# Optimization experiments

Hardware: AMD Instinct MI355X
Metric: run time of the kernel (lower is better)

## Reference

```python
import jax, jax.numpy as jnp
import numpy as np

N = 300_000      # active voxels
L = 128          # occupied bounding grid side
M = 32           # unet width m
CIN = 3          # input_feature_number
NCLASS = 20
K = 27           # 3x3x3 submanifold kernel
BLOCK_REPS = 2
BN_EPS = 1e-4


def _build_neighbors(rng):
    """Rulebook: for each active voxel, index of each of its 27 neighbors (N = missing)."""
    coords = rng.integers(0, L, size=(int(N * 1.5), 3), dtype=np.int64)
    keys = coords[:, 0] * L * L + coords[:, 1] * L + coords[:, 2]
    keys = np.unique(keys)[:N]
    assert keys.shape[0] == N
    x = keys // (L * L); y = (keys // L) % L; z = keys % L
    c = np.stack([x, y, z], 1)                      # [N,3] sorted-by-key coords
    nbr = np.full((N, K), N, dtype=np.int32)
    k = 0
    for dx in (-1, 0, 1):
        for dy in (-1, 0, 1):
            for dz in (-1, 0, 1):
                nc = c + np.array([dx, dy, dz])
                valid = ((nc >= 0) & (nc < L)).all(1)
                nk = nc[:, 0] * L * L + nc[:, 1] * L + nc[:, 2]
                pos = np.searchsorted(keys, nk).clip(0, N - 1)
                found = valid & (keys[pos] == nk)
                nbr[:, k] = np.where(found, pos, N).astype(np.int32)
                k += 1
    return nbr


def setup_inputs() -> dict:
    rng = np.random.default_rng(0)
    nbr_idx = jnp.asarray(_build_neighbors(rng))
    key = jax.random.key(0)
    ks = jax.random.split(key, 16)
    s = 0.1
    inp = {
        "features": jax.random.normal(ks[0], (N, CIN), jnp.float32),
        "nbr_idx": nbr_idx,
        # initial SubmanifoldConvolution(3, m, 3, bias=False)
        "w0": jax.random.normal(ks[1], (K, CIN, M), jnp.float32) * s,
        # residual tower params: [rep, conv_in_block(2), ...]
        "bw": jax.random.normal(ks[2], (BLOCK_REPS, 2, K, M, M), jnp.float32) * s,
        "bg": jnp.ones((BLOCK_REPS, 2, M), jnp.float32),
        "bb": jnp.zeros((BLOCK_REPS, 2, M), jnp.float32),
        # final BatchNormReLU(m)
        "gf": jnp.ones((M,), jnp.float32),
        "bf": jnp.zeros((M,), jnp.float32),
        # dense heads
        "w_cls": jax.random.normal(ks[3], (M, NCLASS), jnp.float32) * s,
        "b_cls": jnp.zeros((NCLASS,), jnp.float32),
        "w_fe": jax.random.normal(ks[4], (M, M), jnp.float32) * s,
        "b_fe": jnp.zeros((M,), jnp.float32),
        "w_le": jax.random.normal(ks[5], (M, M), jnp.float32) * s,
        "b_le": jnp.zeros((M,), jnp.float32),
        "w_fr": jax.random.normal(ks[6], (M, M), jnp.float32) * s,
        "b_fr": jnp.zeros((M,), jnp.float32),
        "w_lr": jax.random.normal(ks[7], (M, 1), jnp.float32) * s,
        "b_lr": jnp.zeros((1,), jnp.float32),
    }
    return inp


def _subconv(feat, nbr, W):
    # feat [N,Cin], nbr [N,27] with sentinel N -> zero row, W [27,Cin,Cout]
    fpad = jnp.concatenate([feat, jnp.zeros((1, feat.shape[1]), feat.dtype)], 0)
    gathered = fpad[nbr]                       # [N,27,Cin] irregular gather
    return jnp.einsum('nkc,kcd->nd', gathered, W)


def _bn(x, g, b):
    mu = x.mean(0)
    var = ((x - mu) ** 2).mean(0)
    return (x - mu) * jax.lax.rsqrt(var + BN_EPS) * g + b


def reference(features, nbr_idx, w0, bw, bg, bb, gf, bf,
              w_cls, b_cls, w_fe, b_fe, w_le, b_le, w_fr, b_fr, w_lr, b_lr):
    feat = _subconv(features, nbr_idx, w0)     # [N,M]
    for r in range(BLOCK_REPS):                # pre-activation residual blocks
        h = _subconv(jax.nn.relu(_bn(feat, bg[r, 0], bb[r, 0])), nbr_idx, bw[r, 0])
        h = _subconv(jax.nn.relu(_bn(h, bg[r, 1], bb[r, 1])), nbr_idx, bw[r, 1])
        feat = feat + h
    feat = jax.nn.relu(_bn(feat, gf, bf))      # BatchNormReLU(m) + OutputLayer
    y = feat @ w_cls + b_cls                                   # [N,20]
    embedding = (feat @ w_fe + b_fe) @ w_le + b_le             # [N,32]
    offset = jax.nn.sigmoid((feat @ w_fr + b_fr) @ w_lr + b_lr)  # [N,1]
    return (y, embedding, offset)
```

## Files before the change

### kernel.cpp

```cpp
#include <hip/hip_runtime.h>

#define NVOX 300000
#define K27 27

typedef __attribute__((ext_vector_type(8))) __bf16 bf16x8;
typedef __attribute__((ext_vector_type(8))) unsigned short ushort8;
typedef __attribute__((ext_vector_type(4))) float f32x4;

__device__ inline unsigned short f2bf(float x){
  unsigned int u = __float_as_uint(x);
  unsigned int r = (u + 0x7FFFu + ((u >> 16) & 1u)) >> 16;
  return (unsigned short)r;
}

__global__ void pack_w_kernel(const float* __restrict__ bw, unsigned short* __restrict__ pw){
  int t = blockIdx.x*256 + threadIdx.x;
  if (t >= 4*K27*2*64) return;
  int l  = t & 63;
  int h  = (t >> 6) & 1;
  int k  = (t >> 7) % K27;
  int cv = t / (128*K27);
  int g = l >> 4, r16 = l & 15;
  ushort8 o;
  #pragma unroll
  for (int i = 0; i < 8; ++i){
    int c  = g*8 + i;
    int oc = h*16 + r16;
    o[i] = f2bf(bw[(((cv*K27 + k)*32) + c)*32 + oc]);
  }
  *reinterpret_cast<ushort8*>(pw + t*8) = o;
}

__global__ void pack_hw_kernel(const float* __restrict__ w_cls, const float* __restrict__ b_cls,
                               const float* __restrict__ w_fe,  const float* __restrict__ b_fe,
                               const float* __restrict__ w_le,
                               const float* __restrict__ w_fr,  const float* __restrict__ b_fr,
                               unsigned short* __restrict__ pwh, float* __restrict__ bcat){
  int t = blockIdx.x*512 + threadIdx.x;
  if (t < 96){
    float v = 0.f;
    if (t < 32)      v = b_fe[t];
    else if (t < 64) v = b_fr[t-32];
    else if (t < 84) v = b_cls[t-64];
    bcat[t] = v;
  }
  if (t >= 8*64) return;
  int l = t & 63, f = t >> 6;
  int g = l >> 4, r16 = l & 15;
  ushort8 o;
  #pragma unroll
  for (int i = 0; i < 8; ++i){
    int k = g*8 + i;
    float v;
    if (f < 6){
      int col = f*16 + r16;
      if (col < 32)      v = w_fe[k*32 + col];
      else if (col < 64) v = w_fr[k*32 + (col-32)];
      else { int c = col - 64; v = (c < 20) ? w_cls[k*20 + c] : 0.f; }
    } else {
      int col = (f-6)*16 + r16;
      v = w_le[k*32 + col];
    }
    o[i] = f2bf(v);
  }
  *reinterpret_cast<ushort8*>(pwh + t*8) = o;
}

__global__ void __launch_bounds__(256) conv0_kernel(
    const float* __restrict__ feats, const int* __restrict__ nbr,
    const float* __restrict__ w0, float* __restrict__ out,
    float* __restrict__ stats){
  __shared__ int   snbr[256*K27];
  __shared__ float trans[256*33];
  __shared__ float sstat[64];
  int tid  = threadIdx.x;
  int base = blockIdx.x * 256;
  for (int i = tid; i < 256*K27; i += 256){
    int v = base + i / K27;
    snbr[i] = (v < NVOX) ? nbr[base*K27 + i] : NVOX;
  }
  if (tid < 64) sstat[tid] = 0.f;
  __syncthreads();

  float acc[32];
  #pragma unroll
  for (int d = 0; d < 32; ++d) acc[d] = 0.f;
  for (int k = 0; k < K27; ++k){
    int j = snbr[tid*K27 + k];
    float f0 = 0.f, f1 = 0.f, f2 = 0.f;
    if (j < NVOX){
      f0 = feats[j*3+0]; f1 = feats[j*3+1]; f2 = feats[j*3+2];
    }
    const float* wk = w0 + k*96;
    #pragma unroll
    for (int d = 0; d < 32; ++d)
      acc[d] += f0*wk[d] + f1*wk[32+d] + f2*wk[64+d];
  }

  #pragma unroll
  for (int d = 0; d < 32; ++d) trans[tid*33 + d] = acc[d];
  __syncthreads();

  {
    int ch = tid & 31, grp = tid >> 5;
    float ps = 0.f, pss = 0.f;
    #pragma unroll 4
    for (int rr = 0; rr < 32; ++rr){
      float v = trans[(grp*32 + rr)*33 + ch];
      ps += v; pss += v*v;
    }
    atomicAdd(&sstat[ch], ps);
    atomicAdd(&sstat[32+ch], pss);
  }

  #pragma unroll
  for (int it = 0; it < 8; ++it){
    int row = it*32 + (tid >> 3);
    int c0  = (tid & 7)*4;
    if (base + row < NVOX){
      float4 v;
      v.x = trans[row*33 + c0+0];
      v.y = trans[row*33 + c0+1];
      v.z = trans[row*33 + c0+2];
      v.w = trans[row*33 + c0+3];
      *reinterpret_cast<float4*>(out + (size_t)(base+row)*32 + c0) = v;
    }
  }
  __syncthreads();
  if (tid < 64) atomicAdd(&stats[(blockIdx.x & 63)*64 + tid], sstat[tid]);
}

__global__ void bn_finalize_kernel(const float* __restrict__ stats,
                                   const float* __restrict__ g, const float* __restrict__ b,
                                   float* __restrict__ bnp){
  int t = threadIdx.x;
  if (t >= 32) return;
  float s = 0.f, q = 0.f;
  for (int i = 0; i < 64; ++i){ s += stats[i*64 + t]; q += stats[i*64 + 32 + t]; }
  float inv = 1.0f / (float)NVOX;
  float mu  = s * inv;
  float var = q * inv - mu*mu;
  float sc  = g[t] * rsqrtf(var + 1e-4f);
  bnp[t]      = sc;
  bnp[32 + t] = b[t] - mu*sc;
}

__global__ void act_kernel(const float* __restrict__ trunk, const float* __restrict__ bnp,
                           unsigned short* __restrict__ act){
  int t = blockIdx.x*256 + threadIdx.x;
  if (t >= (NVOX+1)*4) return;
  int row = t >> 2, part = t & 3;
  ushort8 o;
  if (row < NVOX){
    const float* p = trunk + (size_t)row*32 + part*8;
    #pragma unroll
    for (int i = 0; i < 8; ++i){
      float v = p[i]*bnp[part*8 + i] + bnp[32 + part*8 + i];
      v = fmaxf(v, 0.f);
      o[i] = f2bf(v);
    }
  } else {
    #pragma unroll
    for (int i = 0; i < 8; ++i) o[i] = 0;
  }
  *reinterpret_cast<ushort8*>(act + (size_t)row*32 + part*8) = o;
}

template<bool RES>
__global__ void __launch_bounds__(256) conv_mfma_kernel(
    const unsigned short* __restrict__ act, const int* __restrict__ nbr,
    const unsigned short* __restrict__ pw, float* __restrict__ trunk,
    float* __restrict__ stats){
  __shared__ int   snbr[256*K27];
  __shared__ float sstat[64];
  int tid  = threadIdx.x;
  int base = blockIdx.x*256;
  for (int i = tid; i < 256*K27; i += 256){
    int v = base + i / K27;
    snbr[i] = (v < NVOX) ? nbr[base*K27 + i] : NVOX;
  }
  if (tid < 64) sstat[tid] = 0.f;
  __syncthreads();

  int l = tid & 63, w = tid >> 6;
  int g = l >> 4, r16 = l & 15;
  const int vb = w*64;

  f32x4 acc[4][2];
  #pragma unroll
  for (int t = 0; t < 4; ++t)
    #pragma unroll
    for (int h = 0; h < 2; ++h)
      acc[t][h] = (f32x4){0.f, 0.f, 0.f, 0.f};

  for (int k = 0; k < K27; ++k){
    bf16x8 b0 = *reinterpret_cast<const bf16x8*>(pw + (k*2 + 0)*512 + l*8);
    bf16x8 b1 = *reinterpret_cast<const bf16x8*>(pw + (k*2 + 1)*512 + l*8);
    bf16x8 a[4];
    #pragma unroll
    for (int t = 0; t < 4; ++t){
      int j = snbr[(vb + t*16 + r16)*K27 + k];
      a[t] = *reinterpret_cast<const bf16x8*>(act + (size_t)j*32 + g*8);
    }
    #pragma unroll
    for (int t = 0; t < 4; ++t){
      acc[t][0] = __builtin_amdgcn_mfma_f32_16x16x32_bf16(a[t], b0, acc[t][0], 0, 0, 0);
      acc[t][1] = __builtin_amdgcn_mfma_f32_16x16x32_bf16(a[t], b1, acc[t][1], 0, 0, 0);
    }
  }

  float s0[2] = {0.f, 0.f}, s1[2] = {0.f, 0.f};
  #pragma unroll
  for (int t = 0; t < 4; ++t){
    #pragma unroll
    for (int r = 0; r < 4; ++r){
      int row = base + vb + t*16 + g*4 + r;
      if (row < NVOX){
        #pragma unroll
        for (int h = 0; h < 2; ++h){
          float v = acc[t][h][r];
          float* p = trunk + (size_t)row*32 + h*16 + r16;
          if (RES) v += *p;
          *p = v;
          s0[h] += v; s1[h] += v*v;
        }
      }
    }
  }
  #pragma unroll
  for (int h = 0; h < 2; ++h){
    s0[h] += __shfl_xor(s0[h], 16);
    s0[h] += __shfl_xor(s0[h], 32);
    s1[h] += __shfl_xor(s1[h], 16);
    s1[h] += __shfl_xor(s1[h], 32);
  }
  if (l < 16){
    atomicAdd(&sstat[r16],        s0[0]);
    atomicAdd(&sstat[32 + r16],   s1[0]);
    atomicAdd(&sstat[16 + r16],   s0[1]);
    atomicAdd(&sstat[48 + r16],   s1[1]);
  }
  __syncthreads();
  if (tid < 64) atomicAdd(&stats[(blockIdx.x & 63)*64 + tid], sstat[tid]);
}

__global__ void __launch_bounds__(256) heads_mfma_kernel(
    const float* __restrict__ trunk, const float* __restrict__ bnp,
    const unsigned short* __restrict__ pwh, const float* __restrict__ bcat,
    const float* __restrict__ b_le, const float* __restrict__ w_lr, const float* __restrict__ b_lr,
    float* __restrict__ out){
  __shared__ float lds[4][16][33];
  int tid = threadIdx.x;
  int l = tid & 63, w = tid >> 6;
  int g = l >> 4, r16 = l & 15;
  int base = blockIdx.x*256 + w*64;

  bf16x8 B1[6], B2[2];
  #pragma unroll
  for (int f = 0; f < 6; ++f)
    B1[f] = *reinterpret_cast<const bf16x8*>(pwh + f*512 + l*8);
  #pragma unroll
  for (int h = 0; h < 2; ++h)
    B2[h] = *reinterpret_cast<const bf16x8*>(pwh + (6+h)*512 + l*8);

  float4 sc0 = *reinterpret_cast<const float4*>(bnp + g*8);
  float4 sc1 = *reinterpret_cast<const float4*>(bnp + g*8 + 4);
  float4 bi0 = *reinterpret_cast<const float4*>(bnp + 32 + g*8);
  float4 bi1 = *reinterpret_cast<const float4*>(bnp + 32 + g*8 + 4);
  float wlr0 = w_lr[r16], wlr1 = w_lr[16 + r16];
  float blr  = b_lr[0];
  float bc0  = bcat[r16],      bc1  = bcat[16 + r16];
  float bc2  = bcat[32 + r16], bc3  = bcat[48 + r16];
  float bc4  = bcat[64 + r16], bc5  = bcat[80 + r16];
  float ble0 = b_le[r16],      ble1 = b_le[16 + r16];

  float* out_e = out + (size_t)NVOX*20;
  float* out_o = out + (size_t)NVOX*52;

  for (int t = 0; t < 4; ++t){
    int arow = base + t*16 + r16;
    float4 fa = {0.f,0.f,0.f,0.f}, fb = {0.f,0.f,0.f,0.f};
    if (arow < NVOX){
      fa = *reinterpret_cast<const float4*>(trunk + (size_t)arow*32 + g*8);
      fb = *reinterpret_cast<const float4*>(trunk + (size_t)arow*32 + g*8 + 4);
    }
    ushort8 au;
    au[0] = f2bf(fmaxf(fa.x*sc0.x + bi0.x, 0.f));
    au[1] = f2bf(fmaxf(fa.y*sc0.y + bi0.y, 0.f));
    au[2] = f2bf(fmaxf(fa.z*sc0.z + bi0.z, 0.f));
    au[3] = f2bf(fmaxf(fa.w*sc0.w + bi0.w, 0.f));
    au[4] = f2bf(fmaxf(fb.x*sc1.x + bi1.x, 0.f));
    au[5] = f2bf(fmaxf(fb.y*sc1.y + bi1.y, 0.f));
    au[6] = f2bf(fmaxf(fb.z*sc1.z + bi1.z, 0.f));
    au[7] = f2bf(fmaxf(fb.w*sc1.w + bi1.w, 0.f));
    bf16x8 a = __builtin_bit_cast(bf16x8, au);

    f32x4 acc[6];
    #pragma unroll
    for (int j = 0; j < 6; ++j){
      acc[j] = (f32x4){0.f,0.f,0.f,0.f};
      acc[j] = __builtin_amdgcn_mfma_f32_16x16x32_bf16(a, B1[j], acc[j], 0, 0, 0);
    }

    #pragma unroll
    for (int r = 0; r < 4; ++r){
      int orow = base + t*16 + g*4 + r;
      if (orow < NVOX){
        out[(size_t)orow*20 + r16] = acc[4][r] + bc4;
        if (r16 < 4)
          out[(size_t)orow*20 + 16 + r16] = acc[5][r] + bc5;
      }
    }

    float part[4];
    #pragma unroll
    for (int r = 0; r < 4; ++r)
      part[r] = (acc[2][r] + bc2)*wlr0 + (acc[3][r] + bc3)*wlr1;
    #pragma unroll
    for (int r = 0; r < 4; ++r){
      part[r] += __shfl_xor(part[r], 1);
      part[r] += __shfl_xor(part[r], 2);
      part[r] += __shfl_xor(part[r], 4);
      part[r] += __shfl_xor(part[r], 8);
    }
    if (r16 == 0){
      #pragma unroll
      for (int r = 0; r < 4; ++r){
        int orow = base + t*16 + g*4 + r;
        if (orow < NVOX)
          out_o[orow] = 1.f/(1.f + __expf(-(part[r] + blr)));
      }
    }

    #pragma unroll
    for (int r = 0; r < 4; ++r){
      lds[w][g*4 + r][r16]      = acc[0][r] + bc0;
      lds[w][g*4 + r][16 + r16] = acc[1][r] + bc1;
    }
    __syncthreads();
    ushort8 a2u;
    #pragma unroll
    for (int i = 0; i < 8; ++i)
      a2u[i] = f2bf(lds[w][r16][g*8 + i]);
    bf16x8 a2 = __builtin_bit_cast(bf16x8, a2u);
    f32x4 e0 = (f32x4){0.f,0.f,0.f,0.f}, e1 = (f32x4){0.f,0.f,0.f,0.f};
    e0 = __builtin_amdgcn_mfma_f32_16x16x32_bf16(a2, B2[0], e0, 0, 0, 0);
    e1 = __builtin_amdgcn_mfma_f32_16x16x32_bf16(a2, B2[1], e1, 0, 0, 0);
    #pragma unroll
    for (int r = 0; r < 4; ++r){
      int orow = base + t*16 + g*4 + r;
      if (orow < NVOX){
        out_e[(size_t)orow*32 + r16]      = e0[r] + ble0;
        out_e[(size_t)orow*32 + 16 + r16] = e1[r] + ble1;
      }
    }
    __syncthreads();
  }
}

extern "C" void kernel_launch(void* const* d_in, const int* in_sizes, int n_in,
                              void* d_out, int out_size, void* d_ws, size_t ws_size,
                              hipStream_t stream){
  const float* features = (const float*)d_in[0];
  const int*   nbr      = (const int*)  d_in[1];
  const float* w0       = (const float*)d_in[2];
  const float* bw       = (const float*)d_in[3];
  const float* bg       = (const float*)d_in[4];
  const float* bb       = (const float*)d_in[5];
  const float* gf       = (const float*)d_in[6];
  const float* bf       = (const float*)d_in[7];
  const float* w_cls    = (const float*)d_in[8];
  const float* b_cls    = (const float*)d_in[9];
  const float* w_fe     = (const float*)d_in[10];
  const float* b_fe     = (const float*)d_in[11];
  const float* w_le     = (const float*)d_in[12];
  const float* b_le     = (const float*)d_in[13];
  const float* w_fr     = (const float*)d_in[14];
  const float* b_fr     = (const float*)d_in[15];
  const float* w_lr     = (const float*)d_in[16];
  const float* b_lr     = (const float*)d_in[17];
  float* out = (float*)d_out;

  char* ws = (char*)d_ws;
  float*          trunkA = (float*)(ws);
  float*          trunkH = (float*)(ws + 38400000);
  unsigned short* actB   = (unsigned short*)(ws + 76800000);
  unsigned short* pw     = (unsigned short*)(ws + 96000128);
  float*          stats  = (float*)(ws + 96221312);
  float*          bnp    = (float*)(ws + 96303232);
  unsigned short* pwh    = (unsigned short*)(ws + 96304512);
  float*          bcat   = (float*)(ws + 96312704);

  hipMemsetAsync(stats, 0, 5*64*64*sizeof(float), stream);
  pack_w_kernel<<<(4*K27*2*64 + 255)/256, 256, 0, stream>>>(bw, pw);
  pack_hw_kernel<<<1, 512, 0, stream>>>(w_cls, b_cls, w_fe, b_fe, w_le, w_fr, b_fr, pwh, bcat);

  const int NB = (NVOX + 255)/256;
  const int NA = ((NVOX+1)*4 + 255)/256;

  conv0_kernel<<<NB, 256, 0, stream>>>(features, nbr, w0, trunkA, stats + 0*4096);
  bn_finalize_kernel<<<1, 64, 0, stream>>>(stats + 0*4096, bg +  0, bb +  0, bnp +   0);
  act_kernel<<<NA, 256, 0, stream>>>(trunkA, bnp +   0, actB);
  conv_mfma_kernel<false><<<NB, 256, 0, stream>>>(actB, nbr, pw + 0*27648, trunkH, stats + 1*4096);
  bn_finalize_kernel<<<1, 64, 0, stream>>>(stats + 1*4096, bg + 32, bb + 32, bnp +  64);
  act_kernel<<<NA, 256, 0, stream>>>(trunkH, bnp +  64, actB);
  conv_mfma_kernel<true ><<<NB, 256, 0, stream>>>(actB, nbr, pw + 1*27648, trunkA, stats + 2*4096);
  bn_finalize_kernel<<<1, 64, 0, stream>>>(stats + 2*4096, bg + 64, bb + 64, bnp + 128);
  act_kernel<<<NA, 256, 0, stream>>>(trunkA, bnp + 128, actB);
  conv_mfma_kernel<false><<<NB, 256, 0, stream>>>(actB, nbr, pw + 2*27648, trunkH, stats + 3*4096);
  bn_finalize_kernel<<<1, 64, 0, stream>>>(stats + 3*4096, bg + 96, bb + 96, bnp + 192);
  act_kernel<<<NA, 256, 0, stream>>>(trunkH, bnp + 192, actB);
  conv_mfma_kernel<true ><<<NB, 256, 0, stream>>>(actB, nbr, pw + 3*27648, trunkA, stats + 4*4096);
  bn_finalize_kernel<<<1, 64, 0, stream>>>(stats + 4*4096, gf, bf, bnp + 256);
  heads_mfma_kernel<<<NB, 256, 0, stream>>>(trunkA, bnp + 256, pwh, bcat,
                                            b_le, w_lr, b_lr, out);
}
```

Before: 503.6 us.

## Use MFMA for first conv, fuse BN finalize into consumers, prefetch conv gathers

The scalar first convolution becomes an MFMA kernel. Input features are pre-padded to float4 rows with a zero sentinel, and w0 is packed into bf16 with taps paired along K. The separate single-block BN finalize launches are removed; every block of the activation and heads kernels recomputes the BN scale and bias from the stats buffer. The residual conv loop is fully unrolled with software prefetch of the next tap's gathers and weights. The cost is redundant per-block stats reduction, bf16 rounding of the raw input features, and higher register pressure from unrolling.

```diff
diff --git a/kernel.cpp b/kernel.cpp
--- a/kernel.cpp
+++ b/kernel.cpp
@@ -13,22 +13,41 @@
   return (unsigned short)r;
 }
 
-__global__ void pack_w_kernel(const float* __restrict__ bw, unsigned short* __restrict__ pw){
+__global__ void pack_w_kernel(const float* __restrict__ bw, const float* __restrict__ w0,
+                              unsigned short* __restrict__ pw, unsigned short* __restrict__ pw0){
   int t = blockIdx.x*256 + threadIdx.x;
-  if (t >= 4*K27*2*64) return;
-  int l  = t & 63;
-  int h  = (t >> 6) & 1;
-  int k  = (t >> 7) % K27;
-  int cv = t / (128*K27);
+  if (t < 4*K27*2*64){
+    int l  = t & 63;
+    int h  = (t >> 6) & 1;
+    int k  = (t >> 7) % K27;
+    int cv = t / (128*K27);
+    int g = l >> 4, r16 = l & 15;
+    ushort8 o;
+    #pragma unroll
+    for (int i = 0; i < 8; ++i){
+      int c  = g*8 + i;
+      int oc = h*16 + r16;
+      o[i] = f2bf(bw[(((cv*K27 + k)*32) + c)*32 + oc]);
+    }
+    *reinterpret_cast<ushort8*>(pw + t*8) = o;
+    return;
+  }
+  int u = t - 4*K27*2*64;
+  if (u >= 4*2*64) return;
+  int l  = u & 63;
+  int h  = (u >> 6) & 1;
+  int kb = u >> 7;
   int g = l >> 4, r16 = l & 15;
+  int col = h*16 + r16;
   ushort8 o;
   #pragma unroll
   for (int i = 0; i < 8; ++i){
-    int c  = g*8 + i;
-    int oc = h*16 + r16;
-    o[i] = f2bf(bw[(((cv*K27 + k)*32) + c)*32 + oc]);
-  }
-  *reinterpret_cast<ushort8*>(pw + t*8) = o;
+    int k   = kb*32 + g*8 + i;
+    int tap = k >> 2, ch = k & 3;
+    float v = (tap < K27 && ch < 3) ? w0[(tap*3 + ch)*32 + col] : 0.f;
+    o[i] = f2bf(v);
+  }
+  *reinterpret_cast<ushort8*>(pw0 + u*8) = o;
 }
 
 __global__ void pack_hw_kernel(const float* __restrict__ w_cls, const float* __restrict__ b_cls,
@@ -66,15 +85,24 @@
   *reinterpret_cast<ushort8*>(pwh + t*8) = o;
 }
 
-__global__ void __launch_bounds__(256) conv0_kernel(
-    const float* __restrict__ feats, const int* __restrict__ nbr,
-    const float* __restrict__ w0, float* __restrict__ out,
+__global__ void prepad_kernel(const float* __restrict__ feats, float4* __restrict__ fpad){
+  int row = blockIdx.x*256 + threadIdx.x;
+  if (row > NVOX) return;
+  float4 v = {0.f, 0.f, 0.f, 0.f};
+  if (row < NVOX){
+    v.x = feats[row*3+0]; v.y = feats[row*3+1]; v.z = feats[row*3+2];
+  }
+  fpad[row] = v;
+}
+
+__global__ void __launch_bounds__(256) conv0_mfma_kernel(
+    const float4* __restrict__ fpad, const int* __restrict__ nbr,
+    const unsigned short* __restrict__ pw0, float* __restrict__ trunk,
     float* __restrict__ stats){
   __shared__ int   snbr[256*K27];
-  __shared__ float trans[256*33];
   __shared__ float sstat[64];
   int tid  = threadIdx.x;
-  int base = blockIdx.x * 256;
+  int base = blockIdx.x*256;
   for (int i = tid; i < 256*K27; i += 256){
     int v = base + i / K27;
     snbr[i] = (v < NVOX) ? nbr[base*K27 + i] : NVOX;
@@ -82,72 +110,98 @@
   if (tid < 64) sstat[tid] = 0.f;
   __syncthreads();
 
-  float acc[32];
-  #pragma unroll
-  for (int d = 0; d < 32; ++d) acc[d] = 0.f;
-  for (int k = 0; k < K27; ++k){
-    int j = snbr[tid*K27 + k];
-    float f0 = 0.f, f1 = 0.f, f2 = 0.f;
-    if (j < NVOX){
-      f0 = feats[j*3+0]; f1 = feats[j*3+1]; f2 = feats[j*3+2];
-    }
-    const float* wk = w0 + k*96;
-    #pragma unroll
-    for (int d = 0; d < 32; ++d)
-      acc[d] += f0*wk[d] + f1*wk[32+d] + f2*wk[64+d];
-  }
-
-  #pragma unroll
-  for (int d = 0; d < 32; ++d) trans[tid*33 + d] = acc[d];
-  __syncthreads();
-
-  {
-    int ch = tid & 31, grp = tid >> 5;
-    float ps = 0.f, pss = 0.f;
-    #pragma unroll 4
-    for (int rr = 0; rr < 32; ++rr){
-      float v = trans[(grp*32 + rr)*33 + ch];
-      ps += v; pss += v*v;
-    }
-    atomicAdd(&sstat[ch], ps);
-    atomicAdd(&sstat[32+ch], pss);
-  }
-
-  #pragma unroll
-  for (int it = 0; it < 8; ++it){
-    int row = it*32 + (tid >> 3);
-    int c0  = (tid & 7)*4;
-    if (base + row < NVOX){
-      float4 v;
-      v.x = trans[row*33 + c0+0];
-      v.y = trans[row*33 + c0+1];
-      v.z = trans[row*33 + c0+2];
-      v.w = trans[row*33 + c0+3];
-      *reinterpret_cast<float4*>(out + (size_t)(base+row)*32 + c0) = v;
-    }
+  int l = tid & 63, w = tid >> 6;
+  int g = l >> 4, r16 = l & 15;
+  const int vb = w*64;
+
+  bf16x8 B[4][2];
+  #pragma unroll
+  for (int kb = 0; kb < 4; ++kb)
+    #pragma unroll
+    for (int h = 0; h < 2; ++h)
+      B[kb][h] = *reinterpret_cast<const bf16x8*>(pw0 + (kb*2 + h)*512 + l*8);
+
+  f32x4 acc[4][2];
+  #pragma unroll
+  for (int t = 0; t < 4; ++t)
+    #pragma unroll
+    for (int h = 0; h < 2; ++h)
+      acc[t][h] = (f32x4){0.f,0.f,0.f,0.f};
+
+  #pragma unroll
+  for (int t = 0; t < 4; ++t){
+    int row = (vb + t*16 + r16)*K27;
+    #pragma unroll
+    for (int kb = 0; kb < 4; ++kb){
+      int tap0 = kb*8 + g*2;
+      int tap1 = tap0 + 1;
+      int i0 = (tap0 < K27) ? tap0 : 0;
+      int i1 = (tap1 < K27) ? tap1 : 0;
+      int j0 = snbr[row + i0]; if (tap0 >= K27) j0 = NVOX;
+      int j1 = snbr[row + i1]; if (tap1 >= K27) j1 = NVOX;
+      float4 v0 = fpad[j0];
+      float4 v1 = fpad[j1];
+      ushort8 au;
+      au[0] = f2bf(v0.x); au[1] = f2bf(v0.y); au[2] = f2bf(v0.z); au[3] = 0;
+      au[4] = f2bf(v1.x); au[5] = f2bf(v1.y); au[6] = f2bf(v1.z); au[7] = 0;
+      bf16x8 a = __builtin_bit_cast(bf16x8, au);
+      acc[t][0] = __builtin_amdgcn_mfma_f32_16x16x32_bf16(a, B[kb][0], acc[t][0], 0, 0, 0);
+      acc[t][1] = __builtin_amdgcn_mfma_f32_16x16x32_bf16(a, B[kb][1], acc[t][1], 0, 0, 0);
+    }
+  }
+
+  float s0[2] = {0.f, 0.f}, s1[2] = {0.f, 0.f};
+  #pragma unroll
+  for (int t = 0; t < 4; ++t){
+    #pragma unroll
+    for (int r = 0; r < 4; ++r){
+      int row = base + vb + t*16 + g*4 + r;
+      if (row < NVOX){
+        #pragma unroll
+        for (int h = 0; h < 2; ++h){
+          float v = acc[t][h][r];
+          trunk[(size_t)row*32 + h*16 + r16] = v;
+          s0[h] += v; s1[h] += v*v;
+        }
+      }
+    }
+  }
+  #pragma unroll
+  for (int h = 0; h < 2; ++h){
+    s0[h] += __shfl_xor(s0[h], 16);
+    s0[h] += __shfl_xor(s0[h], 32);
+    s1[h] += __shfl_xor(s1[h], 16);
+    s1[h] += __shfl_xor(s1[h], 32);
+  }
+  if (l < 16){
+    atomicAdd(&sstat[r16],      s0[0]);
+    atomicAdd(&sstat[32 + r16], s1[0]);
+    atomicAdd(&sstat[16 + r16], s0[1]);
+    atomicAdd(&sstat[48 + r16], s1[1]);
   }
   __syncthreads();
   if (tid < 64) atomicAdd(&stats[(blockIdx.x & 63)*64 + tid], sstat[tid]);
 }
 
-__global__ void bn_finalize_kernel(const float* __restrict__ stats,
-                                   const float* __restrict__ g, const float* __restrict__ b,
-                                   float* __restrict__ bnp){
-  int t = threadIdx.x;
-  if (t >= 32) return;
-  float s = 0.f, q = 0.f;
-  for (int i = 0; i < 64; ++i){ s += stats[i*64 + t]; q += stats[i*64 + 32 + t]; }
-  float inv = 1.0f / (float)NVOX;
-  float mu  = s * inv;
-  float var = q * inv - mu*mu;
-  float sc  = g[t] * rsqrtf(var + 1e-4f);
-  bnp[t]      = sc;
-  bnp[32 + t] = b[t] - mu*sc;
-}
-
-__global__ void act_kernel(const float* __restrict__ trunk, const float* __restrict__ bnp,
-                           unsigned short* __restrict__ act){
-  int t = blockIdx.x*256 + threadIdx.x;
+__global__ void __launch_bounds__(256) act_kernel(
+    const float* __restrict__ trunk, const float* __restrict__ stats,
+    const float* __restrict__ g, const float* __restrict__ b,
+    unsigned short* __restrict__ act){
+  __shared__ float sbnp[64];
+  int tid = threadIdx.x;
+  if (tid < 32){
+    float s = 0.f, q = 0.f;
+    for (int i = 0; i < 64; ++i){ s += stats[i*64 + tid]; q += stats[i*64 + 32 + tid]; }
+    float inv = 1.0f / (float)NVOX;
+    float mu  = s * inv;
+    float var = q * inv - mu*mu;
+    float sc  = g[tid] * rsqrtf(var + 1e-4f);
+    sbnp[tid]      = sc;
+    sbnp[32 + tid] = b[tid] - mu*sc;
+  }
+  __syncthreads();
+
+  int t = blockIdx.x*256 + tid;
   if (t >= (NVOX+1)*4) return;
   int row = t >> 2, part = t & 3;
   ushort8 o;
@@ -155,7 +209,7 @@
     const float* p = trunk + (size_t)row*32 + part*8;
     #pragma unroll
     for (int i = 0; i < 8; ++i){
-      float v = p[i]*bnp[part*8 + i] + bnp[32 + part*8 + i];
+      float v = p[i]*sbnp[part*8 + i] + sbnp[32 + part*8 + i];
       v = fmaxf(v, 0.f);
       o[i] = f2bf(v);
     }
@@ -185,28 +239,50 @@
   int l = tid & 63, w = tid >> 6;
   int g = l >> 4, r16 = l & 15;
   const int vb = w*64;
+  const int rb0 = (vb      + r16)*K27;
+  const int rb1 = (vb + 16 + r16)*K27;
+  const int rb2 = (vb + 32 + r16)*K27;
+  const int rb3 = (vb + 48 + r16)*K27;
 
   f32x4 acc[4][2];
   #pragma unroll
   for (int t = 0; t < 4; ++t)
     #pragma unroll
     for (int h = 0; h < 2; ++h)
-      acc[t][h] = (f32x4){0.f, 0.f, 0.f, 0.f};
-
+      acc[t][h] = (f32x4){0.f,0.f,0.f,0.f};
+
+  bf16x8 nb0 = *reinterpret_cast<const bf16x8*>(pw + l*8);
+  bf16x8 nb1 = *reinterpret_cast<const bf16x8*>(pw + 512 + l*8);
+  bf16x8 na0, na1, na2, na3;
+  {
+    int j0 = snbr[rb0], j1 = snbr[rb1], j2 = snbr[rb2], j3 = snbr[rb3];
+    na0 = *reinterpret_cast<const bf16x8*>(act + (size_t)j0*32 + g*8);
+    na1 = *reinterpret_cast<const bf16x8*>(act + (size_t)j1*32 + g*8);
+    na2 = *reinterpret_cast<const bf16x8*>(act + (size_t)j2*32 + g*8);
+    na3 = *reinterpret_cast<const bf16x8*>(act + (size_t)j3*32 + g*8);
+  }
+
+  #pragma unroll
   for (int k = 0; k < K27; ++k){
-    bf16x8 b0 = *reinterpret_cast<const bf16x8*>(pw + (k*2 + 0)*512 + l*8);
-    bf16x8 b1 = *reinterpret_cast<const bf16x8*>(pw + (k*2 + 1)*512 + l*8);
-    bf16x8 a[4];
-    #pragma unroll
-    for (int t = 0; t < 4; ++t){
-      int j = snbr[(vb + t*16 + r16)*K27 + k];
-      a[t] = *reinterpret_cast<const bf16x8*>(act + (size_t)j*32 + g*8);
-    }
-    #pragma unroll
-    for (int t = 0; t < 4; ++t){
-      acc[t][0] = __builtin_amdgcn_mfma_f32_16x16x32_bf16(a[t], b0, acc[t][0], 0, 0, 0);
-      acc[t][1] = __builtin_amdgcn_mfma_f32_16x16x32_bf16(a[t], b1, acc[t][1], 0, 0, 0);
-    }
+    bf16x8 b0 = nb0, b1 = nb1;
+    bf16x8 a0 = na0, a1 = na1, a2 = na2, a3 = na3;
+    if (k + 1 < K27){
+      nb0 = *reinterpret_cast<const bf16x8*>(pw + ((k+1)*2    )*512 + l*8);
+      nb1 = *reinterpret_cast<const bf16x8*>(pw + ((k+1)*2 + 1)*512 + l*8);
+      int j0 = snbr[rb0 + k+1], j1 = snbr[rb1 + k+1], j2 = snbr[rb2 + k+1], j3 = snbr[rb3 + k+1];
+      na0 = *reinterpret_cast<const bf16x8*>(act + (size_t)j0*32 + g*8);
+      na1 = *reinterpret_cast<const bf16x8*>(act + (size_t)j1*32 + g*8);
+      na2 = *reinterpret_cast<const bf16x8*>(act + (size_t)j2*32 + g*8);
+      na3 = *reinterpret_cast<const bf16x8*>(act + (size_t)j3*32 + g*8);
+    }
+    acc[0][0] = __builtin_amdgcn_mfma_f32_16x16x32_bf16(a0, b0, acc[0][0], 0, 0, 0);
+    acc[0][1] = __builtin_amdgcn_mfma_f32_16x16x32_bf16(a0, b1, acc[0][1], 0, 0, 0);
+    acc[1][0] = __builtin_amdgcn_mfma_f32_16x16x32_bf16(a1, b0, acc[1][0], 0, 0, 0);
+    acc[1][1] = __builtin_amdgcn_mfma_f32_16x16x32_bf16(a1, b1, acc[1][1], 0, 0, 0);
+    acc[2][0] = __builtin_amdgcn_mfma_f32_16x16x32_bf16(a2, b0, acc[2][0], 0, 0, 0);
+    acc[2][1] = __builtin_amdgcn_mfma_f32_16x16x32_bf16(a2, b1, acc[2][1], 0, 0, 0);
+    acc[3][0] = __builtin_amdgcn_mfma_f32_16x16x32_bf16(a3, b0, acc[3][0], 0, 0, 0);
+    acc[3][1] = __builtin_amdgcn_mfma_f32_16x16x32_bf16(a3, b1, acc[3][1], 0, 0, 0);
   }
 
   float s0[2] = {0.f, 0.f}, s1[2] = {0.f, 0.f};
@@ -235,22 +311,36 @@
     s1[h] += __shfl_xor(s1[h], 32);
   }
   if (l < 16){
-    atomicAdd(&sstat[r16],        s0[0]);
-    atomicAdd(&sstat[32 + r16],   s1[0]);
-    atomicAdd(&sstat[16 + r16],   s0[1]);
-    atomicAdd(&sstat[48 + r16],   s1[1]);
+    atomicAdd(&sstat[r16],      s0[0]);
+    atomicAdd(&sstat[32 + r16], s1[0]);
+    atomicAdd(&sstat[16 + r16], s0[1]);
+    atomicAdd(&sstat[48 + r16], s1[1]);
   }
   __syncthreads();
   if (tid < 64) atomicAdd(&stats[(blockIdx.x & 63)*64 + tid], sstat[tid]);
 }
 
 __global__ void __launch_bounds__(256) heads_mfma_kernel(
-    const float* __restrict__ trunk, const float* __restrict__ bnp,
+    const float* __restrict__ trunk, const float* __restrict__ stats,
+    const float* __restrict__ gf, const float* __restrict__ bf,
     const unsigned short* __restrict__ pwh, const float* __restrict__ bcat,
     const float* __restrict__ b_le, const float* __restrict__ w_lr, const float* __restrict__ b_lr,
     float* __restrict__ out){
   __shared__ float lds[4][16][33];
+  __shared__ float sbnp[64];
   int tid = threadIdx.x;
+  if (tid < 32){
+    float s = 0.f, q = 0.f;
+    for (int i = 0; i < 64; ++i){ s += stats[i*64 + tid]; q += stats[i*64 + 32 + tid]; }
+    float inv = 1.0f / (float)NVOX;
+    float mu  = s * inv;
+    float var = q * inv - mu*mu;
+    float sc  = gf[tid] * rsqrtf(var + 1e-4f);
+    sbnp[tid]      = sc;
+    sbnp[32 + tid] = bf[tid] - mu*sc;
+  }
+  __syncthreads();
+
   int l = tid & 63, w = tid >> 6;
   int g = l >> 4, r16 = l & 15;
   int base = blockIdx.x*256 + w*64;
@@ -263,10 +353,9 @@
   for (int h = 0; h < 2; ++h)
     B2[h] = *reinterpret_cast<const bf16x8*>(pwh + (6+h)*512 + l*8);
 
-  float4 sc0 = *reinterpret_cast<const float4*>(bnp + g*8);
-  float4 sc1 = *reinterpret_cast<const float4*>(bnp + g*8 + 4);
-  float4 bi0 = *reinterpret_cast<const float4*>(bnp + 32 + g*8);
-  float4 bi1 = *reinterpret_cast<const float4*>(bnp + 32 + g*8 + 4);
+  float sc[8], bi[8];
+  #pragma unroll
+  for (int i = 0; i < 8; ++i){ sc[i] = sbnp[g*8 + i]; bi[i] = sbnp[32 + g*8 + i]; }
   float wlr0 = w_lr[r16], wlr1 = w_lr[16 + r16];
   float blr  = b_lr[0];
   float bc0  = bcat[r16],      bc1  = bcat[16 + r16];
@@ -279,20 +368,20 @@
 
   for (int t = 0; t < 4; ++t){
     int arow = base + t*16 + r16;
-    float4 fa = {0.f,0.f,0.f,0.f}, fb = {0.f,0.f,0.f,0.f};
+    float4 fa = {0.f,0.f,0.f,0.f}, fb2 = {0.f,0.f,0.f,0.f};
     if (arow < NVOX){
-      fa = *reinterpret_cast<const float4*>(trunk + (size_t)arow*32 + g*8);
-      fb = *reinterpret_cast<const float4*>(trunk + (size_t)arow*32 + g*8 + 4);
+      fa  = *reinterpret_cast<const float4*>(trunk + (size_t)arow*32 + g*8);
+      fb2 = *reinterpret_cast<const float4*>(trunk + (size_t)arow*32 + g*8 + 4);
     }
     ushort8 au;
-    au[0] = f2bf(fmaxf(fa.x*sc0.x + bi0.x, 0.f));
-    au[1] = f2bf(fmaxf(fa.y*sc0.y + bi0.y, 0.f));
-    au[2] = f2bf(fmaxf(fa.z*sc0.z + bi0.z, 0.f));
-    au[3] = f2bf(fmaxf(fa.w*sc0.w + bi0.w, 0.f));
-    au[4] = f2bf(fmaxf(fb.x*sc1.x + bi1.x, 0.f));
-    au[5] = f2bf(fmaxf(fb.y*sc1.y + bi1.y, 0.f));
-    au[6] = f2bf(fmaxf(fb.z*sc1.z + bi1.z, 0.f));
-    au[7] = f2bf(fmaxf(fb.w*sc1.w + bi1.w, 0.f));
+    au[0] = f2bf(fmaxf(fa.x*sc[0] + bi[0], 0.f));
+    au[1] = f2bf(fmaxf(fa.y*sc[1] + bi[1], 0.f));
+    au[2] = f2bf(fmaxf(fa.z*sc[2] + bi[2], 0.f));
+    au[3] = f2bf(fmaxf(fa.w*sc[3] + bi[3], 0.f));
+    au[4] = f2bf(fmaxf(fb2.x*sc[4] + bi[4], 0.f));
+    au[5] = f2bf(fmaxf(fb2.y*sc[5] + bi[5], 0.f));
+    au[6] = f2bf(fmaxf(fb2.z*sc[6] + bi[6], 0.f));
+    au[7] = f2bf(fmaxf(fb2.w*sc[7] + bi[7], 0.f));
     bf16x8 a = __builtin_bit_cast(bf16x8, au);
 
     f32x4 acc[6];
@@ -384,34 +473,31 @@
   char* ws = (char*)d_ws;
   float*          trunkA = (float*)(ws);
   float*          trunkH = (float*)(ws + 38400000);
+  float4*         fpad   = (float4*)(ws + 38400000);
   unsigned short* actB   = (unsigned short*)(ws + 76800000);
   unsigned short* pw     = (unsigned short*)(ws + 96000128);
-  float*          stats  = (float*)(ws + 96221312);
-  float*          bnp    = (float*)(ws + 96303232);
-  unsigned short* pwh    = (unsigned short*)(ws + 96304512);
-  float*          bcat   = (float*)(ws + 96312704);
+  unsigned short* pw0    = (unsigned short*)(ws + 96221312);
+  float*          stats  = (float*)(ws + 96229504);
+  unsigned short* pwh    = (unsigned short*)(ws + 96311424);
+  float*          bcat   = (float*)(ws + 96319616);
 
   hipMemsetAsync(stats, 0, 5*64*64*sizeof(float), stream);
-  pack_w_kernel<<<(4*K27*2*64 + 255)/256, 256, 0, stream>>>(bw, pw);
+  pack_w_kernel<<<(4*K27*2*64 + 4*2*64 + 255)/256, 256, 0, stream>>>(bw, w0, pw, pw0);
   pack_hw_kernel<<<1, 512, 0, stream>>>(w_cls, b_cls, w_fe, b_fe, w_le, w_fr, b_fr, pwh, bcat);
+  prepad_kernel<<<(NVOX + 256)/256, 256, 0, stream>>>(features, fpad);
 
   const int NB = (NVOX + 255)/256;
   const int NA = ((NVOX+1)*4 + 255)/256;
 
-  conv0_kernel<<<NB, 256, 0, stream>>>(features, nbr, w0, trunkA, stats + 0*4096);
-  bn_finalize_kernel<<<1, 64, 0, stream>>>(stats + 0*4096, bg +  0, bb +  0, bnp +   0);
-  act_kernel<<<NA, 256, 0, stream>>>(trunkA, bnp +   0, actB);
+  conv0_mfma_kernel<<<NB, 256, 0, stream>>>(fpad, nbr, pw0, trunkA, stats + 0*4096);
+  act_kernel<<<NA, 256, 0, stream>>>(trunkA, stats + 0*4096, bg +  0, bb +  0, actB);
   conv_mfma_kernel<false><<<NB, 256, 0, stream>>>(actB, nbr, pw + 0*27648, trunkH, stats + 1*4096);
-  bn_finalize_kernel<<<1, 64, 0, stream>>>(stats + 1*4096, bg + 32, bb + 32, bnp +  64);
-  act_kernel<<<NA, 256, 0, stream>>>(trunkH, bnp +  64, actB);
+  act_kernel<<<NA, 256, 0, stream>>>(trunkH, stats + 1*4096, bg + 32, bb + 32, actB);
   conv_mfma_kernel<true ><<<NB, 256, 0, stream>>>(actB, nbr, pw + 1*27648, trunkA, stats + 2*4096);
-  bn_finalize_kernel<<<1, 64, 0, stream>>>(stats + 2*4096, bg + 64, bb + 64, bnp + 128);
-  act_kernel<<<NA, 256, 0, stream>>>(trunkA, bnp + 128, actB);
+  act_kernel<<<NA, 256, 0, stream>>>(trunkA, stats + 2*4096, bg + 64, bb + 64, actB);
   conv_mfma_kernel<false><<<NB, 256, 0, stream>>>(actB, nbr, pw + 2*27648, trunkH, stats + 3*4096);
-  bn_finalize_kernel<<<1, 64, 0, stream>>>(stats + 3*4096, bg + 96, bb + 96, bnp + 192);
-  act_kernel<<<NA, 256, 0, stream>>>(trunkH, bnp + 192, actB);
+  act_kernel<<<NA, 256, 0, stream>>>(trunkH, stats + 3*4096, bg + 96, bb + 96, actB);
   conv_mfma_kernel<true ><<<NB, 256, 0, stream>>>(actB, nbr, pw + 3*27648, trunkA, stats + 4*4096);
-  bn_finalize_kernel<<<1, 64, 0, stream>>>(stats + 4*4096, gf, bf, bnp + 256);
-  heads_mfma_kernel<<<NB, 256, 0, stream>>>(trunkA, bnp + 256, pwh, bcat,
+  heads_mfma_kernel<<<NB, 256, 0, stream>>>(trunkA, stats + 4*4096, gf, bf, pwh, bcat,
                                             b_le, w_lr, b_lr, out);
 }
```

Measured after the change: 452.8 us. -10.1%, faster.
